# Performance work log

Hardware: AMD Instinct MI355X
Metric: run time of the kernel (lower is better)

Reference implementation:

```python
import jax, jax.numpy as jnp
import numpy as np

N = 4096
IN_F = 512
OUT_F = 512
EDGE_F = 4


def setup_inputs() -> dict:
    key = jax.random.key(0)
    k1, k2, k3, k4, k5 = jax.random.split(key, 5)
    stdv_w = 1.0 / np.sqrt(OUT_F)
    return {
        "input": jax.random.normal(k1, (N, IN_F), dtype=jnp.float32),
        "adj": jnp.zeros((N, N), dtype=jnp.float32),  # unused by forward (kept for signature fidelity)
        "E": jax.random.normal(k2, (N * N, EDGE_F), dtype=jnp.float32),
        "weight": jax.random.uniform(k3, (IN_F, OUT_F), minval=-stdv_w, maxval=stdv_w, dtype=jnp.float32),
        "weight_q": jax.random.uniform(k4, (EDGE_F, 1), minval=-1.0, maxval=1.0, dtype=jnp.float32),
        "bias": jax.random.uniform(k5, (OUT_F,), minval=-stdv_w, maxval=stdv_w, dtype=jnp.float32),
    }


def reference(input, adj, E, weight, weight_q, bias):
    # support = X @ W : [N, out_f]
    support = input @ weight
    # project per-edge features to scalar edge weights, reshape to dense [N, N] adjacency
    A = (E @ weight_q).reshape(input.shape[0], input.shape[0])
    # propagate: A @ support + bias
    return A @ support + bias
```

## Files before the change

### kernel.cpp

```cpp
#include <hip/hip_runtime.h>
#include <hip/hip_bf16.h>
#include <stdint.h>

#define N_NODES 4096
#define INF_ 512
#define OUTF_ 512

typedef unsigned short u16;
typedef __attribute__((ext_vector_type(8))) short bf16x8;
typedef __attribute__((ext_vector_type(4))) float f32x4;

__device__ __forceinline__ u16 f2bf(float f) {
    union { float f; uint32_t u; } v; v.f = f;
    uint32_t u = v.u;
    uint32_t r = u + 0x7FFFu + ((u >> 16) & 1u);
    return (u16)(r >> 16);
}
__device__ __forceinline__ float bf2f(u16 h) {
    union { uint32_t u; float f; } v; v.u = ((uint32_t)h) << 16;
    return v.f;
}

__device__ __forceinline__ void async16(const void* gsrc, void* ldst) {
    __builtin_amdgcn_global_load_lds(
        (const __attribute__((address_space(1))) unsigned int*)gsrc,
        (__attribute__((address_space(3))) unsigned int*)ldst,
        16, 0, 0);
}

__global__ void prep_kernel(const float4* __restrict__ E4, const float* __restrict__ wq,
                            u16* __restrict__ Abf,
                            const float* __restrict__ X, const float* __restrict__ W,
                            u16* __restrict__ Xbf, u16* __restrict__ WT) {
    const int tid = blockIdx.x * blockDim.x + threadIdx.x;
    const float w0 = wq[0], w1 = wq[1], w2 = wq[2], w3 = wq[3];

    if (tid < N_NODES * INF_) Xbf[tid] = f2bf(X[tid]);
    if (tid < INF_ * OUTF_) {
        int n = tid >> 9, k = tid & 511;
        WT[tid] = f2bf(W[k * OUTF_ + n]);
    }

    const int lane = threadIdx.x & 63;
    const long wave = (long)(tid >> 6);
    const long base = wave * 512;
#pragma unroll
    for (int j = 0; j < 8; ++j) {
        long idx = base + j * 64 + lane;
        float4 e = E4[idx];
        Abf[idx] = f2bf(e.x * w0 + e.y * w1 + e.z * w2 + e.w * w3);
    }
}

__global__ __launch_bounds__(256)
void gemm_support(const u16* __restrict__ A, const u16* __restrict__ B,
                  u16* __restrict__ outT) {
    const int K = 512;
    __shared__ u16 As[64][32];
    __shared__ u16 Bs[128][32];

    const int tid  = threadIdx.x;
    const int lane = tid & 63;
    const int w    = tid >> 6;
    const int wr   = w >> 1;
    const int wc   = w & 1;
    const int brow = blockIdx.x * 64;
    const int bcol = blockIdx.y * 128;

    f32x4 acc[2][4] = {};

    const int srA = w * 16 + (lane >> 2);
    const int srB = w * 32 + (lane >> 2);
    const int sc  = (lane & 3) * 8;

    for (int kt = 0; kt < K; kt += 32) {
        __syncthreads();
        async16(&A[(long)(brow + srA) * K + kt + sc],      &As[w * 16][0]);
        async16(&B[(long)(bcol + srB) * K + kt + sc],      &Bs[w * 32][0]);
        async16(&B[(long)(bcol + srB + 16) * K + kt + sc], &Bs[w * 32 + 16][0]);
        __syncthreads();

        bf16x8 af[2], bfr[4];
#pragma unroll
        for (int m = 0; m < 2; ++m)
            af[m] = *(const bf16x8*)&As[wr * 32 + m * 16 + (lane & 15)][(lane >> 4) * 8];
#pragma unroll
        for (int n = 0; n < 4; ++n)
            bfr[n] = *(const bf16x8*)&Bs[wc * 64 + n * 16 + (lane & 15)][(lane >> 4) * 8];
#pragma unroll
        for (int m = 0; m < 2; ++m)
#pragma unroll
            for (int n = 0; n < 4; ++n)
                acc[m][n] = __builtin_amdgcn_mfma_f32_16x16x32_bf16(af[m], bfr[n], acc[m][n], 0, 0, 0);
    }

#pragma unroll
    for (int m = 0; m < 2; ++m)
#pragma unroll
        for (int n = 0; n < 4; ++n) {
            int col  = bcol + wc * 64 + n * 16 + (lane & 15);
            int row0 = brow + wr * 32 + m * 16 + (lane >> 4) * 4;
#pragma unroll
            for (int r = 0; r < 4; ++r)
                outT[(long)col * N_NODES + row0 + r] = f2bf(acc[m][n][r]);
        }
}

__global__ __launch_bounds__(256)
void gemm2_split(const u16* __restrict__ A, const u16* __restrict__ B,
                 u16* __restrict__ parts) {
    const int K = 4096;
    __shared__ u16 As[128][32];
    __shared__ u16 Bs[128][32];

    const int tid  = threadIdx.x;
    const int lane = tid & 63;
    const int w    = tid >> 6;
    const int wr   = w >> 1;
    const int wc   = w & 1;
    const int brow = blockIdx.x * 128;
    const int bcol = blockIdx.y * 128;
    const int kt0  = blockIdx.z * 512;

    f32x4 acc[4][4] = {};

    const int sr = w * 32 + (lane >> 2);
    const int sc = (lane & 3) * 8;

    for (int kt = kt0; kt < kt0 + 512; kt += 32) {
        __syncthreads();
        async16(&A[(long)(brow + sr) * K + kt + sc],      &As[w * 32][0]);
        async16(&A[(long)(brow + sr + 16) * K + kt + sc], &As[w * 32 + 16][0]);
        async16(&B[(long)(bcol + sr) * K + kt + sc],      &Bs[w * 32][0]);
        async16(&B[(long)(bcol + sr + 16) * K + kt + sc], &Bs[w * 32 + 16][0]);
        __syncthreads();

        bf16x8 af[4], bfr[4];
#pragma unroll
        for (int m = 0; m < 4; ++m)
            af[m] = *(const bf16x8*)&As[wr * 64 + m * 16 + (lane & 15)][(lane >> 4) * 8];
#pragma unroll
        for (int n = 0; n < 4; ++n)
            bfr[n] = *(const bf16x8*)&Bs[wc * 64 + n * 16 + (lane & 15)][(lane >> 4) * 8];
#pragma unroll
        for (int m = 0; m < 4; ++m)
#pragma unroll
            for (int n = 0; n < 4; ++n)
                acc[m][n] = __builtin_amdgcn_mfma_f32_16x16x32_bf16(af[m], bfr[n], acc[m][n], 0, 0, 0);
    }

    u16* outP = parts + (long)blockIdx.z * (N_NODES * OUTF_);
#pragma unroll
    for (int m = 0; m < 4; ++m)
#pragma unroll
        for (int n = 0; n < 4; ++n) {
            int col  = bcol + wc * 64 + n * 16 + (lane & 15);
            int row0 = brow + wr * 64 + m * 16 + (lane >> 4) * 4;
#pragma unroll
            for (int r = 0; r < 4; ++r)
                outP[(long)(row0 + r) * OUTF_ + col] = f2bf(acc[m][n][r]);
        }
}

__global__ void reduce8_kernel(const u16* __restrict__ parts, const float* __restrict__ bias,
                               float* __restrict__ out) {
    const int t = blockIdx.x * blockDim.x + threadIdx.x;
    const long base = (long)t * 8;
    const int col0 = (int)(base & (OUTF_ - 1));
    const long stride = (long)N_NODES * OUTF_;

    float s[8];
#pragma unroll
    for (int j = 0; j < 8; ++j) s[j] = bias[col0 + j];
#pragma unroll
    for (int z = 0; z < 8; ++z) {
        bf16x8 v = *(const bf16x8*)(parts + z * stride + base);
#pragma unroll
        for (int j = 0; j < 8; ++j) s[j] += bf2f((u16)v[j]);
    }
    float4* o4 = (float4*)(out + base);
    o4[0] = make_float4(s[0], s[1], s[2], s[3]);
    o4[1] = make_float4(s[4], s[5], s[6], s[7]);
}

extern "C" void kernel_launch(void* const* d_in, const int* in_sizes, int n_in,
                              void* d_out, int out_size, void* d_ws, size_t ws_size,
                              hipStream_t stream) {
    const float* X    = (const float*)d_in[0];
    const float* E    = (const float*)d_in[2];
    const float* W    = (const float*)d_in[3];
    const float* wq   = (const float*)d_in[4];
    const float* bias = (const float*)d_in[5];
    float* out = (float*)d_out;

    char* ws = (char*)d_ws;
    u16* ST    = (u16*)ws;
    u16* Xbf   = (u16*)(ws + (4l << 20));
    u16* WT    = (u16*)(ws + (8l << 20));
    u16* Abf   = (u16*)(ws + (9l << 20));
    u16* parts = (u16*)(ws + (41l << 20));

    prep_kernel<<<8192, 256, 0, stream>>>((const float4*)E, wq, Abf, X, W, Xbf, WT);
    gemm_support<<<dim3(64, 4), 256, 0, stream>>>(Xbf, WT, ST);
    gemm2_split<<<dim3(32, 4, 8), 256, 0, stream>>>(Abf, ST, parts);
    reduce8_kernel<<<1024, 256, 0, stream>>>(parts, bias, out);
}
```

Before: 110.3 us.

## Fuse edge-feature projection into propagation GEMM A-tile loading

Removes the separate pass that projects E into a bf16 dense adjacency. The propagation GEMM now reads fp32 edge features directly, projects them with weight_q, and writes bf16 values into a padded shared-memory A tile. This avoids writing and rereading the intermediate adjacency matrix. The cost is that each column block rereads the large fp32 E tensor, and the A-tile loads become synchronous register loads instead of async LDS loads.

Result: slower. 149.0 us (+35.1%).

```diff
diff --git a/kernel.cpp b/kernel.cpp
--- a/kernel.cpp
+++ b/kernel.cpp
@@ -28,27 +28,13 @@
         16, 0, 0);
 }
 
-__global__ void prep_kernel(const float4* __restrict__ E4, const float* __restrict__ wq,
-                            u16* __restrict__ Abf,
-                            const float* __restrict__ X, const float* __restrict__ W,
-                            u16* __restrict__ Xbf, u16* __restrict__ WT) {
-    const int tid = blockIdx.x * blockDim.x + threadIdx.x;
-    const float w0 = wq[0], w1 = wq[1], w2 = wq[2], w3 = wq[3];
-
+__global__ void convert_kernel(const float* __restrict__ X, const float* __restrict__ W,
+                               u16* __restrict__ Xbf, u16* __restrict__ WT) {
+    int tid = blockIdx.x * blockDim.x + threadIdx.x;
     if (tid < N_NODES * INF_) Xbf[tid] = f2bf(X[tid]);
     if (tid < INF_ * OUTF_) {
         int n = tid >> 9, k = tid & 511;
         WT[tid] = f2bf(W[k * OUTF_ + n]);
-    }
-
-    const int lane = threadIdx.x & 63;
-    const long wave = (long)(tid >> 6);
-    const long base = wave * 512;
-#pragma unroll
-    for (int j = 0; j < 8; ++j) {
-        long idx = base + j * 64 + lane;
-        float4 e = E4[idx];
-        Abf[idx] = f2bf(e.x * w0 + e.y * w1 + e.z * w2 + e.w * w3);
     }
 }
 
@@ -107,10 +93,10 @@
 }
 
 __global__ __launch_bounds__(256)
-void gemm2_split(const u16* __restrict__ A, const u16* __restrict__ B,
-                 u16* __restrict__ parts) {
+void gemm2_fusedE(const float4* __restrict__ E4, const float* __restrict__ wq,
+                  const u16* __restrict__ B, u16* __restrict__ parts) {
     const int K = 4096;
-    __shared__ u16 As[128][32];
+    __shared__ u16 As[128][40];
     __shared__ u16 Bs[128][32];
 
     const int tid  = threadIdx.x;
@@ -122,17 +108,33 @@
     const int bcol = blockIdx.y * 128;
     const int kt0  = blockIdx.z * 512;
 
+    const float w0 = wq[0], w1 = wq[1], w2 = wq[2], w3 = wq[3];
+
     f32x4 acc[4][4] = {};
 
-    const int sr = w * 32 + (lane >> 2);
-    const int sc = (lane & 3) * 8;
-
-    for (int kt = kt0; kt < kt0 + 512; kt += 32) {
-        __syncthreads();
-        async16(&A[(long)(brow + sr) * K + kt + sc],      &As[w * 32][0]);
-        async16(&A[(long)(brow + sr + 16) * K + kt + sc], &As[w * 32 + 16][0]);
-        async16(&B[(long)(bcol + sr) * K + kt + sc],      &Bs[w * 32][0]);
-        async16(&B[(long)(bcol + sr + 16) * K + kt + sc], &Bs[w * 32 + 16][0]);
+    const int srB = w * 32 + (lane >> 2);
+    const int scB = (lane & 3) * 8;
+    const int erow = tid >> 5;
+    const int ek   = tid & 31;
+
+    for (int it = 0; it < 16; ++it) {
+        const int kt = kt0 + it * 32;
+        __syncthreads();
+        async16(&B[(long)(bcol + srB) * K + kt + scB],      &Bs[w * 32][0]);
+        async16(&B[(long)(bcol + srB + 16) * K + kt + scB], &Bs[w * 32 + 16][0]);
+        float4 ev[8];
+#pragma unroll
+        for (int j = 0; j < 8; ++j)
+            ev[j] = E4[(long)(brow + j * 8 + erow) * N_NODES + kt + ek];
+#pragma unroll
+        for (int j = 0; j < 8; ++j)
+            As[j * 8 + erow][ek] = f2bf(ev[j].x * w0 + ev[j].y * w1 + ev[j].z * w2 + ev[j].w * w3);
+#pragma unroll
+        for (int j = 0; j < 8; ++j)
+            ev[j] = E4[(long)(brow + 64 + j * 8 + erow) * N_NODES + kt + ek];
+#pragma unroll
+        for (int j = 0; j < 8; ++j)
+            As[64 + j * 8 + erow][ek] = f2bf(ev[j].x * w0 + ev[j].y * w1 + ev[j].z * w2 + ev[j].w * w3);
         __syncthreads();
 
         bf16x8 af[4], bfr[4];
@@ -197,11 +199,10 @@
     u16* ST    = (u16*)ws;
     u16* Xbf   = (u16*)(ws + (4l << 20));
     u16* WT    = (u16*)(ws + (8l << 20));
-    u16* Abf   = (u16*)(ws + (9l << 20));
-    u16* parts = (u16*)(ws + (41l << 20));
-
-    prep_kernel<<<8192, 256, 0, stream>>>((const float4*)E, wq, Abf, X, W, Xbf, WT);
+    u16* parts = (u16*)(ws + (9l << 20));
+
+    convert_kernel<<<8192, 256, 0, stream>>>(X, W, Xbf, WT);
     gemm_support<<<dim3(64, 4), 256, 0, stream>>>(Xbf, WT, ST);
-    gemm2_split<<<dim3(32, 4, 8), 256, 0, stream>>>(Abf, ST, parts);
+    gemm2_fusedE<<<dim3(32, 4, 8), 256, 0, stream>>>((const float4*)E, wq, ST, parts);
     reduce8_kernel<<<1024, 256, 0, stream>>>(parts, bias, out);
 }
```

## Overlap chunked edge-weight prep with split-K GEMM slices in mixed kernels

Applied to the files above, without the earlier changes.

Splits the E projection into four column chunks and fuses each chunk's conversion into the same launch as the GEMM blocks for already-prepared K-slices. The support GEMM also shares a launch with the first chunk. The aim is to hide the bandwidth-bound prep behind MFMA compute and use wider vector stores for the bf16 adjacency. The cost is more launches and heterogeneous blocks, and shared memory grows for the support blocks.

Result: slower. 124.9 us (+13.2%).

```diff
diff --git a/kernel.cpp b/kernel.cpp
--- a/kernel.cpp
+++ b/kernel.cpp
@@ -28,47 +28,48 @@
         16, 0, 0);
 }
 
-__global__ void prep_kernel(const float4* __restrict__ E4, const float* __restrict__ wq,
-                            u16* __restrict__ Abf,
-                            const float* __restrict__ X, const float* __restrict__ W,
-                            u16* __restrict__ Xbf, u16* __restrict__ WT) {
-    const int tid = blockIdx.x * blockDim.x + threadIdx.x;
-    const float w0 = wq[0], w1 = wq[1], w2 = wq[2], w3 = wq[3];
-
+__global__ void convert_kernel(const float* __restrict__ X, const float* __restrict__ W,
+                               u16* __restrict__ Xbf, u16* __restrict__ WT) {
+    int tid = blockIdx.x * blockDim.x + threadIdx.x;
     if (tid < N_NODES * INF_) Xbf[tid] = f2bf(X[tid]);
     if (tid < INF_ * OUTF_) {
         int n = tid >> 9, k = tid & 511;
         WT[tid] = f2bf(W[k * OUTF_ + n]);
     }
-
-    const int lane = threadIdx.x & 63;
-    const long wave = (long)(tid >> 6);
-    const long base = wave * 512;
-#pragma unroll
-    for (int j = 0; j < 8; ++j) {
-        long idx = base + j * 64 + lane;
-        float4 e = E4[idx];
-        Abf[idx] = f2bf(e.x * w0 + e.y * w1 + e.z * w2 + e.w * w3);
-    }
-}
-
-__global__ __launch_bounds__(256)
-void gemm_support(const u16* __restrict__ A, const u16* __restrict__ B,
-                  u16* __restrict__ outT) {
+}
+
+__device__ __forceinline__ void prep_body(const float4* __restrict__ E4,
+                                          const float* __restrict__ wq,
+                                          u16* __restrict__ Abf, int chunk, int pb) {
+    const float w0 = wq[0], w1 = wq[1], w2 = wq[2], w3 = wq[3];
+    const long gt  = (long)pb * 256 + threadIdx.x;
+    const long f   = gt * 8;
+    const int row  = (int)(f >> 10);
+    const int c4   = (int)(f & 1023);
+    const float4* src = E4 + (long)row * 4096 + chunk * 1024 + c4;
+    float4 ev[8];
+#pragma unroll
+    for (int j = 0; j < 8; ++j) ev[j] = src[j];
+    union { bf16x8 v; u16 h[8]; } pk;
+#pragma unroll
+    for (int j = 0; j < 8; ++j)
+        pk.h[j] = f2bf(ev[j].x * w0 + ev[j].y * w1 + ev[j].z * w2 + ev[j].w * w3);
+    *(bf16x8*)(Abf + (long)row * 4096 + chunk * 1024 + c4) = pk.v;
+}
+
+__device__ __forceinline__ void support_body(u16 (*As)[32], u16 (*Bs)[32],
+                                             const u16* __restrict__ A, const u16* __restrict__ B,
+                                             u16* __restrict__ outT, int sx, int sy) {
     const int K = 512;
-    __shared__ u16 As[64][32];
-    __shared__ u16 Bs[128][32];
-
     const int tid  = threadIdx.x;
     const int lane = tid & 63;
     const int w    = tid >> 6;
     const int wr   = w >> 1;
     const int wc   = w & 1;
-    const int brow = blockIdx.x * 64;
-    const int bcol = blockIdx.y * 128;
+    const int brow = sx * 64;
+    const int bcol = sy * 128;
 
     f32x4 acc[2][4] = {};
-
     const int srA = w * 16 + (lane >> 2);
     const int srB = w * 32 + (lane >> 2);
     const int sc  = (lane & 3) * 8;
@@ -106,24 +107,20 @@
         }
 }
 
-__global__ __launch_bounds__(256)
-void gemm2_split(const u16* __restrict__ A, const u16* __restrict__ B,
-                 u16* __restrict__ parts) {
+__device__ __forceinline__ void gemm_body(u16 (*As)[32], u16 (*Bs)[32],
+                                          const u16* __restrict__ A, const u16* __restrict__ B,
+                                          u16* __restrict__ parts, int bx, int by, int slice) {
     const int K = 4096;
-    __shared__ u16 As[128][32];
-    __shared__ u16 Bs[128][32];
-
     const int tid  = threadIdx.x;
     const int lane = tid & 63;
     const int w    = tid >> 6;
     const int wr   = w >> 1;
     const int wc   = w & 1;
-    const int brow = blockIdx.x * 128;
-    const int bcol = blockIdx.y * 128;
-    const int kt0  = blockIdx.z * 512;
+    const int brow = bx * 128;
+    const int bcol = by * 128;
+    const int kt0  = slice * 512;
 
     f32x4 acc[4][4] = {};
-
     const int sr = w * 32 + (lane >> 2);
     const int sc = (lane & 3) * 8;
 
@@ -149,7 +146,7 @@
                 acc[m][n] = __builtin_amdgcn_mfma_f32_16x16x32_bf16(af[m], bfr[n], acc[m][n], 0, 0, 0);
     }
 
-    u16* outP = parts + (long)blockIdx.z * (N_NODES * OUTF_);
+    u16* outP = parts + (long)slice * (N_NODES * OUTF_);
 #pragma unroll
     for (int m = 0; m < 4; ++m)
 #pragma unroll
@@ -160,6 +157,36 @@
             for (int r = 0; r < 4; ++r)
                 outP[(long)(row0 + r) * OUTF_ + col] = f2bf(acc[m][n][r]);
         }
+}
+
+__global__ __launch_bounds__(256)
+void mixed0(const u16* __restrict__ Xbf, const u16* __restrict__ WT, u16* __restrict__ ST,
+            const float4* __restrict__ E4, const float* __restrict__ wq, u16* __restrict__ Abf) {
+    __shared__ u16 As[128][32];
+    __shared__ u16 Bs[128][32];
+    const int g = blockIdx.x;
+    if (g < 256) {
+        support_body(As, Bs, Xbf, WT, ST, g & 63, g >> 6);
+    } else {
+        prep_body(E4, wq, Abf, 0, g - 256);
+    }
+}
+
+__global__ __launch_bounds__(256)
+void mixedZ(const float4* __restrict__ E4, const float* __restrict__ wq,
+            u16* __restrict__ Abf, const u16* __restrict__ ST,
+            u16* __restrict__ parts, int gz, int pz) {
+    __shared__ u16 As[128][32];
+    __shared__ u16 Bs[128][32];
+    const int g = blockIdx.x;
+    if (g < 256) {
+        const int bx  = g & 31;
+        const int by  = (g >> 5) & 3;
+        const int sub = g >> 7;
+        gemm_body(As, Bs, Abf, ST, parts, bx, by, gz * 2 + sub);
+    } else if (pz < 4) {
+        prep_body(E4, wq, Abf, pz, g - 256);
+    }
 }
 
 __global__ void reduce8_kernel(const u16* __restrict__ parts, const float* __restrict__ bias,
@@ -200,8 +227,13 @@
     u16* Abf   = (u16*)(ws + (9l << 20));
     u16* parts = (u16*)(ws + (41l << 20));
 
-    prep_kernel<<<8192, 256, 0, stream>>>((const float4*)E, wq, Abf, X, W, Xbf, WT);
-    gemm_support<<<dim3(64, 4), 256, 0, stream>>>(Xbf, WT, ST);
-    gemm2_split<<<dim3(32, 4, 8), 256, 0, stream>>>(Abf, ST, parts);
+    const float4* E4 = (const float4*)E;
+
+    convert_kernel<<<8192, 256, 0, stream>>>(X, W, Xbf, WT);
+    mixed0<<<2304, 256, 0, stream>>>(Xbf, WT, ST, E4, wq, Abf);
+    mixedZ<<<2304, 256, 0, stream>>>(E4, wq, Abf, ST, parts, 0, 1);
+    mixedZ<<<2304, 256, 0, stream>>>(E4, wq, Abf, ST, parts, 1, 2);
+    mixedZ<<<2304, 256, 0, stream>>>(E4, wq, Abf, ST, parts, 2, 3);
+    mixedZ<<<256,  256, 0, stream>>>(E4, wq, Abf, ST, parts, 3, 4);
     reduce8_kernel<<<1024, 256, 0, stream>>>(parts, bias, out);
 }
```
